# Kernel optimization log

Measured on AMD Instinct MI355X. Metric: run time of the kernel, lower is better.

## Reference

```python
import jax, jax.numpy as jnp
import numpy as np

B, T, J = 8, 1024, 25
D_MODEL, D_STATE, D_CONV, EXPAND = 256, 16, 4, 2
D_INNER = EXPAND * D_MODEL            # 512
DT_RANK = (D_MODEL + 15) // 16        # 16
N_CLASSES = 60


def layernorm(x, g, b, eps=1e-5):
    mu = x.mean(-1, keepdims=True)
    var = ((x - mu) ** 2).mean(-1, keepdims=True)
    return (x - mu) * jax.lax.rsqrt(var + eps) * g + b


def selective_scan(u, delta, A, Bm, Cm, D):
    # u, delta: [b,l,d]; A: [d,n]; Bm, Cm: [b,l,n]; D: [d]
    dA = jnp.exp(delta[..., None] * A)                              # [b,l,d,n]
    dBu = delta[..., None] * Bm[:, :, None, :] * u[..., None]        # [b,l,d,n]

    def step(h, inp):
        dA_t, dBu_t, C_t = inp
        h = dA_t * h + dBu_t                                         # [b,d,n]
        y = jnp.einsum('bdn,bn->bd', h, C_t)
        return h, y

    h0 = jnp.zeros((u.shape[0], u.shape[2], A.shape[1]), u.dtype)
    _, ys = jax.lax.scan(step, h0, (jnp.moveaxis(dA, 1, 0),
                                    jnp.moveaxis(dBu, 1, 0),
                                    jnp.moveaxis(Cm, 1, 0)))
    return jnp.moveaxis(ys, 0, 1) + u * D                            # [b,l,d]


def setup_inputs() -> dict:
    key = jax.random.key(0)
    ks = jax.random.split(key, 12)
    rn = lambda k, s, sc=0.02: jax.random.normal(k, s, jnp.float32) * sc
    A_log = jnp.log(jnp.tile(jnp.arange(1, D_STATE + 1, dtype=jnp.float32), (D_INNER, 1)))
    return {
        'x': jax.random.normal(ks[0], (B, T, J, 3), jnp.float32),
        'embed_w': rn(ks[1], (D_MODEL, J * 9)), 'embed_b': jnp.zeros((D_MODEL,), jnp.float32),
        'pre_g': jnp.ones((D_MODEL,), jnp.float32), 'pre_b': jnp.zeros((D_MODEL,), jnp.float32),
        'in_proj_w': rn(ks[2], (2 * D_INNER, D_MODEL)),
        'conv_w': rn(ks[3], (D_INNER, 1, D_CONV)), 'conv_b': jnp.zeros((D_INNER,), jnp.float32),
        'x_proj_w': rn(ks[4], (DT_RANK + 2 * D_STATE, D_INNER)),
        'dt_proj_w': rn(ks[5], (D_INNER, DT_RANK)), 'dt_proj_b': rn(ks[6], (D_INNER,), 0.1),
        'A_log': A_log, 'D': jnp.ones((D_INNER,), jnp.float32),
        'out_proj_w': rn(ks[7], (D_MODEL, D_INNER)),
        'post_g': jnp.ones((D_MODEL,), jnp.float32), 'post_b': jnp.zeros((D_MODEL,), jnp.float32),
        'fine_w': rn(ks[8], (N_CLASSES, D_MODEL)), 'fine_b': jnp.zeros((N_CLASSES,), jnp.float32),
    }


def reference(x, embed_w, embed_b, pre_g, pre_b, in_proj_w, conv_w, conv_b,
              x_proj_w, dt_proj_w, dt_proj_b, A_log, D, out_proj_w,
              post_g, post_b, fine_w, fine_b):
    b, t = x.shape[0], x.shape[1]
    # --- SkeletonNormalizer: root-center (scale_joints=None) ---
    pos = x[..., :3] - x[:, :, 0:1, :3]                              # [B,T,J,3]
    # --- MotionFeatureBuilder: pos / vel / acc ---
    vel = jnp.concatenate([jnp.zeros_like(pos[:, :1]), pos[:, 1:] - pos[:, :-1]], axis=1)
    acc = jnp.concatenate([jnp.zeros_like(vel[:, :1]), vel[:, 1:] - vel[:, :-1]], axis=1)
    feat = jnp.concatenate([pos, vel, acc], axis=-1).reshape(b, t, -1)  # [B,T,J*9]
    # --- embed ---
    feat = feat @ embed_w.T + embed_b                                # [B,T,D_MODEL]
    # --- Mamba block on pre-norm, residual add ---
    hn = layernorm(feat, pre_g, pre_b)
    xz = hn @ in_proj_w.T                                            # [B,T,2*D_INNER]
    xm, res = jnp.split(xz, 2, axis=-1)
    # depthwise causal conv1d over time
    xm = jax.lax.conv_general_dilated(
        jnp.swapaxes(xm, 1, 2), conv_w, (1,), [(D_CONV - 1, 0)],
        dimension_numbers=('NCH', 'OIH', 'NCH'), feature_group_count=D_INNER)
    xm = jnp.swapaxes(xm + conv_b[None, :, None], 1, 2)              # [B,T,D_INNER]
    xm = jax.nn.silu(xm)
    dbl = xm @ x_proj_w.T                                            # [B,T,DT_RANK+2*D_STATE]
    dt = dbl[..., :DT_RANK]
    Bm = dbl[..., DT_RANK:DT_RANK + D_STATE]
    Cm = dbl[..., DT_RANK + D_STATE:]
    delta = jax.nn.softplus(dt @ dt_proj_w.T + dt_proj_b)            # [B,T,D_INNER]
    A = -jnp.exp(A_log)                                              # [D_INNER,D_STATE]
    y = selective_scan(xm, delta, A, Bm, Cm, D)
    y = y * jax.nn.silu(res)
    y = y @ out_proj_w.T                                             # [B,T,D_MODEL]
    feat = feat + y
    # --- post norm, mean pool, classify ---
    feat = layernorm(feat, post_g, post_b)
    pooled = feat.mean(axis=1)                                       # [B,D_MODEL]
    return pooled @ fine_w.T + fine_b                                # [B,N_CLASSES]
```

## Files before the change

kernel.cpp:

```cpp
#include <hip/hip_runtime.h>
#include <hip/hip_bf16.h>
#include <math.h>

#define Bb 8
#define Tt 1024
#define Jj 25
#define D_MODEL 256
#define D_STATE 16
#define D_CONV 4
#define D_INNER 512
#define DT_RANK 16
#define N_CLASSES 60
#define Mrows (Bb*Tt)
#define NC 64
#define CL 16

typedef unsigned short u16;
using bf16x8 = __attribute__((ext_vector_type(8))) __bf16;
using f32x4  = __attribute__((ext_vector_type(4))) float;

__device__ inline u16 f2bf(float x) {
    unsigned u = __float_as_uint(x);
    unsigned r = (u + 0x7fffu + ((u >> 16) & 1u)) >> 16;
    return (u16)r;
// ... 111 lines not shown
#pragma unroll
            for (int in = 0; in < 2; in++)
                acc[im][in] = mfma3(aH[im], aL[im], bH[in], bL[in], acc[im][in]);
    }

    float bias_c[2], g_c[2], b_c[2];
#pragma unroll
    for (int in = 0; in < 2; in++) {
        int gn = nb + in * 16 + fr;
        bias_c[in] = bias[gn];
        g_c[in] = g[gn];
        b_c[in] = b[gn];
    }
#pragma unroll
    for (int im = 0; im < 2; im++)
#pragma unroll
        for (int in = 0; in < 2; in++)
#pragma unroll
            for (int reg = 0; reg < 4; reg++) {
                float v = acc[im][in][reg] + bias_c[in];
                acc[im][in][reg] = v;
                int gm = m0 + im * 16 + quad * 4 + reg;
                int gn = nb + in * 16 + fr;
                feat[(long)gm * 256 + gn] = v;
            }
#pragma unroll
    for (int im = 0; im < 2; im++)
#pragma unroll
        for (int reg = 0; reg < 4; reg++) {
            float p = acc[im][0][reg] + acc[im][1][reg];
            p += __shfl_xor(p, 1);
            p += __shfl_xor(p, 2);
            p += __shfl_xor(p, 4);
            p += __shfl_xor(p, 8);
            if (fr == 0) red[(im * 16 + quad * 4 + reg) * 8 + wave] = p;
        }
    __syncthreads();
    if (tid < BM) {
        float s = 0.f;
#pragma unroll
        for (int i = 0; i < 8; i++) s += red[tid * 8 + i];
        mu_s[tid] = s * (1.f / 256.f);
    }
    __syncthreads();
#pragma unroll
    for (int im = 0; im < 2; im++)
#pragma unroll
        for (int reg = 0; reg < 4; reg++) {
            int rl = im * 16 + quad * 4 + reg;
            float m = mu_s[rl];
            float d0 = acc[im][0][reg] - m, d1 = acc[im][1][reg] - m;
            float p = d0 * d0 + d1 * d1;
            p += __shfl_xor(p, 1);
            p += __shfl_xor(p, 2);
            p += __shfl_xor(p, 4);
            p += __shfl_xor(p, 8);
            if (fr == 0) red[rl * 8 + wave] = p;
        }
    __syncthreads();
    if (tid < BM) {
        float s = 0.f;
#pragma unroll
        for (int i = 0; i < 8; i++) s += red[tid * 8 + i];
        rs_s[tid] = rsqrtf(s * (1.f / 256.f) + 1e-5f);
    }
    __syncthreads();
#pragma unroll
    for (int im = 0; im < 2; im++)
#pragma unroll
        for (int in = 0; in < 2; in++)
#pragma unroll
            for (int reg = 0; reg < 4; reg++) {
                int rl = im * 16 + quad * 4 + reg;
                int gm = m0 + rl;
                int gn = nb + in * 16 + fr;
                float o = (acc[im][in][reg] - mu_s[rl]) * rs_s[rl] * g_c[in] + b_c[in];
                u16 hh, ll;
                split2(o, hh, ll);
                hnh[(long)gm * 256 + gn] = hh;
                hnl[(long)gm * 256 + gn] = ll;
            }
}

__global__ __launch_bounds__(512) void outproj_ln_pool_kernel(
    const u16* __restrict__ Ahi, const u16* __restrict__ Alo,
    const u16* __restrict__ Whi, const u16* __restrict__ Wlo,
    const float* __restrict__ resid,
    const float* __restrict__ g, const float* __restrict__ b,
    float* __restrict__ bp)
{
    constexpr int BM = 32, SW = 520;
    __shared__ u16 AsH[BM * SW], AsL[BM * SW];
    __shared__ float red[BM * 8];
    __shared__ float mu_s[BM], rs_s[BM];
    int tid = threadIdx.x;
    int m0 = blockIdx.x * BM;
    int lane = tid & 63, wave = tid >> 6;
    int fr = lane & 15, quad = lane >> 4;

    for (int s = tid; s < BM * 64; s += 512) {
        int row = s >> 6, seg = s & 63;
        long off = (long)(m0 + row) * 512 + seg * 8;
        *(uint4*)&AsH[row * SW + seg * 8] = *(const uint4*)(Ahi + off);
        *(uint4*)&AsL[row * SW + seg * 8] = *(const uint4*)(Alo + off);
    }
    __syncthreads();

    f32x4 acc[2][2] = {};
    int nb = wave * 32;
#pragma unroll 4
    for (int k0 = 0; k0 < 512; k0 += 32) {
        bf16x8 aH[2], aL[2], bH[2], bL[2];
#pragma unroll
        for (int im = 0; im < 2; im++) {
            int r = im * 16 + fr;
            aH[im] = *(const bf16x8*)&AsH[r * SW + k0 + quad * 8];
            aL[im] = *(const bf16x8*)&AsL[r * SW + k0 + quad * 8];
        }
#pragma unroll
        for (int in = 0; in < 2; in++) {
            long off = (long)(nb + in * 16 + fr) * 512 + k0 + quad * 8;
            bH[in] = *(const bf16x8*)(Whi + off);
            bL[in] = *(const bf16x8*)(Wlo + off);
        }
#pragma unroll
        for (int im = 0; im < 2; im++)
#pragma unroll
            for (int in = 0; in < 2; in++)
                acc[im][in] = mfma3(aH[im], aL[im], bH[in], bL[in], acc[im][in]);
    }

    float g_c[2], b_c[2];
#pragma unroll
    for (int in = 0; in < 2; in++) {
        int gn = nb + in * 16 + fr;
        g_c[in] = g[gn];
        b_c[in] = b[gn];
    }
#pragma unroll
    for (int im = 0; im < 2; im++)
#pragma unroll
        for (int in = 0; in < 2; in++)
#pragma unroll
            for (int reg = 0; reg < 4; reg++) {
                int gm = m0 + im * 16 + quad * 4 + reg;
                int gn = nb + in * 16 + fr;
                acc[im][in][reg] += resid[(long)gm * 256 + gn];
            }
#pragma unroll
    for (int im = 0; im < 2; im++)
#pragma unroll
        for (int reg = 0; reg < 4; reg++) {
            float p = acc[im][0][reg] + acc[im][1][reg];
            p += __shfl_xor(p, 1);
            p += __shfl_xor(p, 2);
            p += __shfl_xor(p, 4);
            p += __shfl_xor(p, 8);
            if (fr == 0) red[(im * 16 + quad * 4 + reg) * 8 + wave] = p;
        }
    __syncthreads();
    if (tid < BM) {
        float s = 0.f;
#pragma unroll
        for (int i = 0; i < 8; i++) s += red[tid * 8 + i];
        mu_s[tid] = s * (1.f / 256.f);
    }
    __syncthreads();
#pragma unroll
    for (int im = 0; im < 2; im++)
#pragma unroll
        for (int reg = 0; reg < 4; reg++) {
            int rl = im * 16 + quad * 4 + reg;
            float m = mu_s[rl];
            float d0 = acc[im][0][reg] - m, d1 = acc[im][1][reg] - m;
            float p = d0 * d0 + d1 * d1;
            p += __shfl_xor(p, 1);
            p += __shfl_xor(p, 2);
            p += __shfl_xor(p, 4);
            p += __shfl_xor(p, 8);
            if (fr == 0) red[rl * 8 + wave] = p;
        }
    __syncthreads();
    if (tid < BM) {
        float s = 0.f;
#pragma unroll
        for (int i = 0; i < 8; i++) s += red[tid * 8 + i];
        rs_s[tid] = rsqrtf(s * (1.f / 256.f) + 1e-5f);
    }
    __syncthreads();
#pragma unroll
    for (int in = 0; in < 2; in++) {
        float cs = 0.f;
#pragma unroll
        for (int im = 0; im < 2; im++)
#pragma unroll
            for (int reg = 0; reg < 4; reg++) {
                int rl = im * 16 + quad * 4 + reg;
                cs += (acc[im][in][reg] - mu_s[rl]) * rs_s[rl] * g_c[in] + b_c[in];
            }
        cs += __shfl_xor(cs, 16);
        cs += __shfl_xor(cs, 32);
        if (quad == 0) {
            int gn = nb + in * 16 + fr;
            atomicAdd(&bp[(long)(m0 >> 6) * 256 + gn], cs);
        }
    }
}

template<int BM, int BN, int EPI>
__global__ __launch_bounds__(256) void gemm_mfma(
    const u16* __restrict__ Ahi, const u16* __restrict__ Alo, int lda,
    const u16* __restrict__ Whi, const u16* __restrict__ Wlo, int ldw,
    const float* __restrict__ bias, const float* __restrict__ resid, int ldr,
    float* __restrict__ C, int ldc, int M, int N, int K)
{
    constexpr int TM = BM / 32;
    constexpr int TN = BN / 32;
    constexpr int SA = 40;
    __shared__ u16 AsH[BM * SA], AsL[BM * SA];
    __shared__ u16 WsH[BN * SA], WsL[BN * SA];
    int tid = threadIdx.x;
    int m0 = blockIdx.y * BM;
    int n0 = blockIdx.x * BN;
    int lane = tid & 63;
    int wave = tid >> 6;
    int wm = wave >> 1, wn = wave & 1;
    int fr = lane & 15, quad = lane >> 4;
    f32x4 acc[TM][TN] = {};

    for (int k0 = 0; k0 < K; k0 += 32) {
        for (int s = tid; s < BM * 4; s += 256) {
            int row = s >> 2, seg = s & 3;
            long off = (long)(m0 + row) * lda + k0 + seg * 8;
            *(uint4*)&AsH[row * SA + seg * 8] = *(const uint4*)(Ahi + off);
            *(uint4*)&AsL[row * SA + seg * 8] = *(const uint4*)(Alo + off);
        }
        for (int s = tid; s < BN * 4; s += 256) {
            int row = s >> 2, seg = s & 3;
            long off = (long)(n0 + row) * ldw + k0 + seg * 8;
            *(uint4*)&WsH[row * SA + seg * 8] = *(const uint4*)(Whi + off);
            *(uint4*)&WsL[row * SA + seg * 8] = *(const uint4*)(Wlo + off);
        }
        __syncthreads();
        bf16x8 aH[TM], aL[TM], bH[TN], bL[TN];
#pragma unroll
        for (int im = 0; im < TM; im++) {
            int r = wm * (BM / 2) + im * 16 + fr;
            aH[im] = *(const bf16x8*)&AsH[r * SA + quad * 8];
            aL[im] = *(const bf16x8*)&AsL[r * SA + quad * 8];
        }
#pragma unroll
        for (int in = 0; in < TN; in++) {
            int r = wn * (BN / 2) + in * 16 + fr;
            bH[in] = *(const bf16x8*)&WsH[r * SA + quad * 8];
            bL[in] = *(const bf16x8*)&WsL[r * SA + quad * 8];
        }
#pragma unroll
        for (int im = 0; im < TM; im++)
#pragma unroll
            for (int in = 0; in < TN; in++)
                acc[im][in] = mfma3(aH[im], aL[im], bH[in], bL[in], acc[im][in]);
        __syncthreads();
    }
#pragma unroll
    for (int im = 0; im < TM; im++) {
#pragma unroll
        for (int in = 0; in < TN; in++) {
#pragma unroll
            for (int reg = 0; reg < 4; reg++) {
                int gm = m0 + wm * (BM / 2) + im * 16 + quad * 4 + reg;
                int gn = n0 + wn * (BN / 2) + in * 16 + fr;
                float v = acc[im][in][reg];
                if (EPI == 1) v += bias[gn];
                if (EPI == 3) v += resid[(long)gm * ldr + gn];
                C[(long)gm * ldc + gn] = v;
            }
        }
    }
}

__global__ __launch_bounds__(512) void scan_p1f(
    const float* __restrict__ xz,
    const float* __restrict__ cw, const float* __restrict__ cb,
    const u16* __restrict__ Whi, const u16* __restrict__ Wlo,
    const float* __restrict__ dtw, const float* __restrict__ dtb,
    const float* __restrict__ A_log,
    float* __restrict__ chunkS, float* __restrict__ sumdelta)
{
    constexpr int SW = 520;
    __shared__ u16 AsH[CL * SW], AsL[CL * SW];
    __shared__ float ds[CL * 48];
    int b = blockIdx.x, c = blockIdx.y, d = threadIdx.x;
    int lane = d & 63, wave = d >> 6;
    int fr = lane & 15, quad = lane >> 4;
    long r0 = (long)b * Tt + (long)c * CL;
    int t0 = c * CL;

    float4 w4 = *(const float4*)(cw + d * 4);
    float cbd = cb[d];
    const float* xc = xz + r0 * 1024 + d;
    float h1 = (t0 >= 1) ? xc[-1024] : 0.f;
    float h2 = (t0 >= 2) ? xc[-2048] : 0.f;
    float h3 = (t0 >= 3) ? xc[-3072] : 0.f;
#pragma unroll
    for (int t = 0; t < CL; t++) {
        float cur = xc[t * 1024];
        float a = cbd + w4.w * cur + w4.z * h1 + w4.y * h2 + w4.x * h3;
        float s = a / (1.f + __expf(-a));
        u16 hh, ll;
        split2(s, hh, ll);
        AsH[t * SW + d] = hh;
        AsL[t * SW + d] = ll;
        h3 = h2; h2 = h1; h1 = cur;
    }
    float Arow[16];
#pragma unroll
    for (int n = 0; n < 16; n++) Arow[n] = -expf(A_log[d * 16 + n]);
    float4 wd[4];
#pragma unroll
    for (int q = 0; q < 4; q++) wd[q] = *(const float4*)(dtw + d * 16 + q * 4);
    float bdt = dtb[d];
    __syncthreads();

    if (wave < 3) {
        f32x4 acc = {};
#pragma unroll
        for (int k0 = 0; k0 < 512; k0 += 32) {
            bf16x8 aH = *(const bf16x8*)&AsH[fr * SW + k0 + quad * 8];
            bf16x8 aL = *(const bf16x8*)&AsL[fr * SW + k0 + quad * 8];
            long off = (long)(wave * 16 + fr) * 512 + k0 + quad * 8;
            bf16x8 bH = *(const bf16x8*)(Whi + off);
            bf16x8 bL = *(const bf16x8*)(Wlo + off);
            acc = mfma3(aH, aL, bH, bL, acc);
        }
#pragma unroll
        for (int reg = 0; reg < 4; reg++)
            ds[(quad * 4 + reg) * 48 + wave * 16 + fr] = acc[reg];
    }
    __syncthreads();

    float S[16];
#pragma unroll
    for (int n = 0; n < 16; n++) S[n] = 0.f;
    float sd = 0.f;
    for (int t = 0; t < CL; t++) {
        const float* row = ds + t * 48;
        float4 t1 = *(const float4*)(row + 0);
        float4 t2 = *(const float4*)(row + 4);
        float4 t3 = *(const float4*)(row + 8);
        float4 t4 = *(const float4*)(row + 12);
        float s = bdt;
        s += t1.x * wd[0].x + t1.y * wd[0].y + t1.z * wd[0].z + t1.w * wd[0].w;
        s += t2.x * wd[1].x + t2.y * wd[1].y + t2.z * wd[1].z + t2.w * wd[1].w;
        s += t3.x * wd[2].x + t3.y * wd[2].y + t3.z * wd[2].z + t3.w * wd[2].w;
        s += t4.x * wd[3].x + t4.y * wd[3].y + t4.z * wd[3].z + t4.w * wd[3].w;
        float dl = softplus_fast(s);
        float u = bf2f(AsH[t * SW + d]) + bf2f(AsL[t * SW + d]);
        float du = dl * u;
        sd += dl;
        float Bn[16];
#pragma unroll
        for (int q = 0; q < 4; q++) {
            float4 bv = *(const float4*)(row + 16 + q * 4);
            Bn[q*4+0] = bv.x; Bn[q*4+1] = bv.y; Bn[q*4+2] = bv.z; Bn[q*4+3] = bv.w;
        }
#pragma unroll
        for (int n = 0; n < 16; n++) {
            float a = __expf(dl * Arow[n]);
            S[n] = a * S[n] + du * Bn[n];
        }
    }
    long base = ((long)(b * NC + c) * 16) * 512 + d;
#pragma unroll
    for (int n = 0; n < 16; n++) chunkS[base + (long)n * 512] = S[n];
    sumdelta[(long)(b * NC + c) * 512 + d] = sd;
}

__global__ __launch_bounds__(256) void scan_combine(float* chunkS,
                                                    const float* __restrict__ sumdelta,
                                                    const float* __restrict__ A_log) {
    int idx = blockIdx.x * 256 + threadIdx.x;
    int d = idx & 511;
    int n = (idx >> 9) & 15;
    int b = idx >> 13;
    float Aval = -expf(A_log[d * 16 + n]);
    float h = 0.f;
    for (int c = 0; c < NC; c++) {
        long si = ((long)(b * NC + c) * 16 + n) * 512 + d;
        float s = chunkS[si];
        float a = __expf(Aval * sumdelta[(long)(b * NC + c) * 512 + d]);
        chunkS[si] = h;
        h = a * h + s;
    }
}

__global__ __launch_bounds__(512) void scan_p2f(
    const float* __restrict__ xz,
    const float* __restrict__ cw, const float* __restrict__ cb,
    const u16* __restrict__ Whi, const u16* __restrict__ Wlo,
    const float* __restrict__ dtw, const float* __restrict__ dtb,
    const float* __restrict__ A_log, const float* __restrict__ Dv,
    const float* __restrict__ chunkH,
    u16* __restrict__ yh, u16* __restrict__ yl)
{
    constexpr int SW = 520;
    __shared__ u16 AsH[CL * SW], AsL[CL * SW];
    __shared__ float ds[CL * 48];
    int b = blockIdx.x, c = blockIdx.y, d = threadIdx.x;
    int lane = d & 63, wave = d >> 6;
    int fr = lane & 15, quad = lane >> 4;
    long r0 = (long)b * Tt + (long)c * CL;
    int t0 = c * CL;

    float4 w4 = *(const float4*)(cw + d * 4);
    float cbd = cb[d];
    const float* xc = xz + r0 * 1024 + d;
    float h1 = (t0 >= 1) ? xc[-1024] : 0.f;
    float h2 = (t0 >= 2) ? xc[-2048] : 0.f;
    float h3 = (t0 >= 3) ? xc[-3072] : 0.f;
#pragma unroll
    for (int t = 0; t < CL; t++) {
        float cur = xc[t * 1024];
        float a = cbd + w4.w * cur + w4.z * h1 + w4.y * h2 + w4.x * h3;
        float s = a / (1.f + __expf(-a));
        u16 hh, ll;
        split2(s, hh, ll);
        AsH[t * SW + d] = hh;
        AsL[t * SW + d] = ll;
        h3 = h2; h2 = h1; h1 = cur;
    }
    float Arow[16];
#pragma unroll
    for (int n = 0; n < 16; n++) Arow[n] = -expf(A_log[d * 16 + n]);
    float4 wd[4];
#pragma unroll
    for (int q = 0; q < 4; q++) wd[q] = *(const float4*)(dtw + d * 16 + q * 4);
    float bdt = dtb[d];
    float Dd = Dv[d];
    float h[16];
    long base = ((long)(b * NC + c) * 16) * 512 + d;
#pragma unroll
    for (int n = 0; n < 16; n++) h[n] = chunkH[base + (long)n * 512];
    __syncthreads();

    if (wave < 3) {
        f32x4 acc = {};
#pragma unroll
        for (int k0 = 0; k0 < 512; k0 += 32) {
            bf16x8 aH = *(const bf16x8*)&AsH[fr * SW + k0 + quad * 8];
            bf16x8 aL = *(const bf16x8*)&AsL[fr * SW + k0 + quad * 8];
            long off = (long)(wave * 16 + fr) * 512 + k0 + quad * 8;
            bf16x8 bH = *(const bf16x8*)(Whi + off);
            bf16x8 bL = *(const bf16x8*)(Wlo + off);
            acc = mfma3(aH, aL, bH, bL, acc);
        }
#pragma unroll
        for (int reg = 0; reg < 4; reg++)
            ds[(quad * 4 + reg) * 48 + wave * 16 + fr] = acc[reg];
    }
    __syncthreads();

    const float* xres = xz + r0 * 1024 + 512 + d;
    for (int t = 0; t < CL; t++) {
        const float* row = ds + t * 48;
        float4 t1 = *(const float4*)(row + 0);
        float4 t2 = *(const float4*)(row + 4);
        float4 t3 = *(const float4*)(row + 8);
        float4 t4 = *(const float4*)(row + 12);
        float s = bdt;
        s += t1.x * wd[0].x + t1.y * wd[0].y + t1.z * wd[0].z + t1.w * wd[0].w;
        s += t2.x * wd[1].x + t2.y * wd[1].y + t2.z * wd[1].z + t2.w * wd[1].w;
        s += t3.x * wd[2].x + t3.y * wd[2].y + t3.z * wd[2].z + t3.w * wd[2].w;
        s += t4.x * wd[3].x + t4.y * wd[3].y + t4.z * wd[3].z + t4.w * wd[3].w;
        float dl = softplus_fast(s);
        float u = bf2f(AsH[t * SW + d]) + bf2f(AsL[t * SW + d]);
        float res = xres[t * 1024];
        float du = dl * u;
        float Bn[16], Cn[16];
#pragma unroll
        for (int q = 0; q < 4; q++) {
            float4 bv = *(const float4*)(row + 16 + q * 4);
            float4 cv = *(const float4*)(row + 32 + q * 4);
            Bn[q*4+0] = bv.x; Bn[q*4+1] = bv.y; Bn[q*4+2] = bv.z; Bn[q*4+3] = bv.w;
            Cn[q*4+0] = cv.x; Cn[q*4+1] = cv.y; Cn[q*4+2] = cv.z; Cn[q*4+3] = cv.w;
        }
        float ysum = 0.f;
#pragma unroll
        for (int n = 0; n < 16; n++) {
            float a = __expf(dl * Arow[n]);
            h[n] = a * h[n] + du * Bn[n];
            ysum += h[n] * Cn[n];
        }
        float yy = ysum + u * Dd;
        float sres = res / (1.f + __expf(-res));
        float outv = yy * sres;
        u16 hh, ll;
        split2(outv, hh, ll);
        long r = r0 + t;
        yh[r * 512 + d] = hh;
        yl[r * 512 + d] = ll;
    }
}

__global__ __launch_bounds__(256) void head_kernel(const float* __restrict__ bp,
                                                   const float* __restrict__ fw,
                                                   const float* __restrict__ fb,
                                                   float* __restrict__ out) {
    __shared__ float pld[256];
    int b = blockIdx.x;
    int d = threadIdx.x;
    float s = 0.f;
#pragma unroll
    for (int i = 0; i < 16; i++)
        s += bp[(long)(b * 16 + i) * 256 + d];
    pld[d] = s;
    __syncthreads();
    if (d < N_CLASSES) {
        float acc = 0.f;
        for (int k = 0; k < 256; k++) acc += pld[k] * fw[d * 256 + k];
        out[b * N_CLASSES + d] = acc * (1.f / (float)Tt) + fb[d];
    }
}

extern "C" void kernel_launch(void* const* d_in, const int* in_sizes, int n_in,
                              void* d_out, int out_size, void* d_ws, size_t ws_size,
                              hipStream_t stream) {
    const float* x         = (const float*)d_in[0];
    const float* embed_w   = (const float*)d_in[1];
    const float* embed_b   = (const float*)d_in[2];
    const float* pre_g     = (const float*)d_in[3];
    const float* pre_b     = (const float*)d_in[4];
    const float* in_proj_w = (const float*)d_in[5];
    const float* conv_w    = (const float*)d_in[6];
    const float* conv_b    = (const float*)d_in[7];
    const float* x_proj_w  = (const float*)d_in[8];
    const float* dt_proj_w = (const float*)d_in[9];
    const float* dt_proj_b = (const float*)d_in[10];
    const float* A_log     = (const float*)d_in[11];
    const float* Dv        = (const float*)d_in[12];
    const float* out_proj_w= (const float*)d_in[13];
    const float* post_g    = (const float*)d_in[14];
    const float* post_b    = (const float*)d_in[15];
    const float* fine_w    = (const float*)d_in[16];
    const float* fine_b    = (const float*)d_in[17];
    float* out = (float*)d_out;
    char* base = (char*)d_ws;

    float* feat     = (float*)(base + 0);
    float* xz       = (float*)(base + 8388608);
    float* chunkS   = (float*)(base + 41943040);
    u16*   xmh      = (u16*)  (base + 58720256);
    u16*   xml      = (u16*)  (base + 67108864);
    u16*   fbh      = (u16*)  (base + 75497472);
    u16*   fbl      = (u16*)  (base + 79691776);
    float* sumdelta = (float*)(base + 85458944);
    float* blockpart= (float*)(base + 86507520);
    u16*   ebh      = (u16*)  (base + 86638592);
    u16*   ebl      = ebh + 65536;
    u16*   iph      = ebl + 65536;
    u16*   ipl      = iph + 262144;
    u16*   xph      = ipl + 262144;
    u16*   xpl      = xph + 24576;
    u16*   oph      = xpl + 24576;
    u16*   opl      = oph + 131072;

    prep_kernel<<<dim3(1888 + 128), dim3(256), 0, stream>>>(
        embed_w, in_proj_w, x_proj_w, out_proj_w,
        ebh, ebl, iph, ipl, xph, xpl, oph, opl, blockpart);

    embed_ln_kernel<<<dim3(Mrows / 32), dim3(512), 0, stream>>>(
        x, ebh, ebl, embed_b, pre_g, pre_b, feat, fbh, fbl);

    gemm_mfma<128,64,0><<<dim3(16, 64), dim3(256), 0, stream>>>(
        fbh, fbl, 256, iph, ipl, 256, nullptr, nullptr, 0, xz, 1024, Mrows, 1024, 256);

    scan_p1f<<<dim3(Bb, NC), dim3(512), 0, stream>>>(
        xz, conv_w, conv_b, xph, xpl, dt_proj_w, dt_proj_b, A_log,
        chunkS, sumdelta);
    scan_combine<<<dim3(256), dim3(256), 0, stream>>>(chunkS, sumdelta, A_log);
    scan_p2f<<<dim3(Bb, NC), dim3(512), 0, stream>>>(
        xz, conv_w, conv_b, xph, xpl, dt_proj_w, dt_proj_b, A_log, Dv,
        chunkS, xmh, xml);

    outproj_ln_pool_kernel<<<dim3(Mrows / 32), dim3(512), 0, stream>>>(
        xmh, xml, oph, opl, feat, post_g, post_b, blockpart);

    head_kernel<<<dim3(Bb), dim3(256), 0, stream>>>(blockpart, fine_w, fine_b, out);
}
```

Before: 236.0 us.

## Replace generic in_proj GEMM with full-K A-tile kernel streaming weights from global

Swaps the templated tiled GEMM for in_proj for a dedicated kernel. Each block loads a 64x256 activation tile (hi and lo bf16 halves) into LDS once, with a single barrier. Waves then read weight fragments straight from global memory, which removes the per-K-step LDS staging and the syncs between steps. The weights are small and likely cache-resident. The risk is that the global weight loads sit on the MFMA critical path without prefetching, and the larger LDS footprint limits occupancy.

```diff
diff --git a/kernel.cpp b/kernel.cpp
--- a/kernel.cpp
+++ b/kernel.cpp
@@ -217,6 +217,63 @@
             }
 }
 
+__global__ __launch_bounds__(512, 2) void inproj_kernel(
+    const u16* __restrict__ Ahi, const u16* __restrict__ Alo,
+    const u16* __restrict__ Whi, const u16* __restrict__ Wlo,
+    float* __restrict__ xz)
+{
+    constexpr int BM = 64, SW = 264;
+    __shared__ u16 AsH[BM * SW], AsL[BM * SW];
+    int tid = threadIdx.x;
+    int n0 = blockIdx.x * 256;
+    int m0 = blockIdx.y * BM;
+    int lane = tid & 63, wave = tid >> 6;
+    int fr = lane & 15, quad = lane >> 4;
+
+    for (int s = tid; s < BM * 32; s += 512) {
+        int row = s >> 5, seg = s & 31;
+        long off = (long)(m0 + row) * 256 + seg * 8;
+        *(uint4*)&AsH[row * SW + seg * 8] = *(const uint4*)(Ahi + off);
+        *(uint4*)&AsL[row * SW + seg * 8] = *(const uint4*)(Alo + off);
+    }
+    __syncthreads();
+
+    f32x4 acc[4][2] = {};
+    int nb = n0 + wave * 32;
+#pragma unroll
+    for (int k0 = 0; k0 < 256; k0 += 32) {
+        bf16x8 aH[4], aL[4], bH[2], bL[2];
+#pragma unroll
+        for (int im = 0; im < 4; im++) {
+            int r = im * 16 + fr;
+            aH[im] = *(const bf16x8*)&AsH[r * SW + k0 + quad * 8];
+            aL[im] = *(const bf16x8*)&AsL[r * SW + k0 + quad * 8];
+        }
+#pragma unroll
+        for (int in = 0; in < 2; in++) {
+            long off = (long)(nb + in * 16 + fr) * 256 + k0 + quad * 8;
+            bH[in] = *(const bf16x8*)(Whi + off);
+            bL[in] = *(const bf16x8*)(Wlo + off);
+        }
+#pragma unroll
+        for (int im = 0; im < 4; im++)
+#pragma unroll
+            for (int in = 0; in < 2; in++)
+                acc[im][in] = mfma3(aH[im], aL[im], bH[in], bL[in], acc[im][in]);
+    }
+
+#pragma unroll
+    for (int im = 0; im < 4; im++)
+#pragma unroll
+        for (int in = 0; in < 2; in++)
+#pragma unroll
+            for (int reg = 0; reg < 4; reg++) {
+                int gm = m0 + im * 16 + quad * 4 + reg;
+                int gn = nb + in * 16 + fr;
+                xz[(long)gm * 1024 + gn] = acc[im][in][reg];
+            }
+}
+
 __global__ __launch_bounds__(512) void outproj_ln_pool_kernel(
     const u16* __restrict__ Ahi, const u16* __restrict__ Alo,
     const u16* __restrict__ Whi, const u16* __restrict__ Wlo,
@@ -338,78 +395,6 @@
         if (quad == 0) {
             int gn = nb + in * 16 + fr;
             atomicAdd(&bp[(long)(m0 >> 6) * 256 + gn], cs);
-        }
-    }
-}
-
-template<int BM, int BN, int EPI>
-__global__ __launch_bounds__(256) void gemm_mfma(
-    const u16* __restrict__ Ahi, const u16* __restrict__ Alo, int lda,
-    const u16* __restrict__ Whi, const u16* __restrict__ Wlo, int ldw,
-    const float* __restrict__ bias, const float* __restrict__ resid, int ldr,
-    float* __restrict__ C, int ldc, int M, int N, int K)
-{
-    constexpr int TM = BM / 32;
-    constexpr int TN = BN / 32;
-    constexpr int SA = 40;
-    __shared__ u16 AsH[BM * SA], AsL[BM * SA];
-    __shared__ u16 WsH[BN * SA], WsL[BN * SA];
-    int tid = threadIdx.x;
-    int m0 = blockIdx.y * BM;
-    int n0 = blockIdx.x * BN;
-    int lane = tid & 63;
-    int wave = tid >> 6;
-    int wm = wave >> 1, wn = wave & 1;
-    int fr = lane & 15, quad = lane >> 4;
-    f32x4 acc[TM][TN] = {};
-
-    for (int k0 = 0; k0 < K; k0 += 32) {
-        for (int s = tid; s < BM * 4; s += 256) {
-            int row = s >> 2, seg = s & 3;
-            long off = (long)(m0 + row) * lda + k0 + seg * 8;
-            *(uint4*)&AsH[row * SA + seg * 8] = *(const uint4*)(Ahi + off);
-            *(uint4*)&AsL[row * SA + seg * 8] = *(const uint4*)(Alo + off);
-        }
-        for (int s = tid; s < BN * 4; s += 256) {
-            int row = s >> 2, seg = s & 3;
-            long off = (long)(n0 + row) * ldw + k0 + seg * 8;
-            *(uint4*)&WsH[row * SA + seg * 8] = *(const uint4*)(Whi + off);
-            *(uint4*)&WsL[row * SA + seg * 8] = *(const uint4*)(Wlo + off);
-        }
-        __syncthreads();
-        bf16x8 aH[TM], aL[TM], bH[TN], bL[TN];
-#pragma unroll
-        for (int im = 0; im < TM; im++) {
-            int r = wm * (BM / 2) + im * 16 + fr;
-            aH[im] = *(const bf16x8*)&AsH[r * SA + quad * 8];
-            aL[im] = *(const bf16x8*)&AsL[r * SA + quad * 8];
-        }
-#pragma unroll
-        for (int in = 0; in < TN; in++) {
-            int r = wn * (BN / 2) + in * 16 + fr;
-            bH[in] = *(const bf16x8*)&WsH[r * SA + quad * 8];
-            bL[in] = *(const bf16x8*)&WsL[r * SA + quad * 8];
-        }
-#pragma unroll
-        for (int im = 0; im < TM; im++)
-#pragma unroll
-            for (int in = 0; in < TN; in++)
-                acc[im][in] = mfma3(aH[im], aL[im], bH[in], bL[in], acc[im][in]);
-        __syncthreads();
-    }
-#pragma unroll
-    for (int im = 0; im < TM; im++) {
-#pragma unroll
-        for (int in = 0; in < TN; in++) {
-#pragma unroll
-            for (int reg = 0; reg < 4; reg++) {
-                int gm = m0 + wm * (BM / 2) + im * 16 + quad * 4 + reg;
-                int gn = n0 + wn * (BN / 2) + in * 16 + fr;
-                float v = acc[im][in][reg];
-                if (EPI == 1) v += bias[gn];
-                if (EPI == 3) v += resid[(long)gm * ldr + gn];
-                C[(long)gm * ldc + gn] = v;
-            }
         }
     }
 }
@@ -706,8 +691,8 @@
     embed_ln_kernel<<<dim3(Mrows / 32), dim3(512), 0, stream>>>(
         x, ebh, ebl, embed_b, pre_g, pre_b, feat, fbh, fbl);
 
-    gemm_mfma<128,64,0><<<dim3(16, 64), dim3(256), 0, stream>>>(
-        fbh, fbl, 256, iph, ipl, 256, nullptr, nullptr, 0, xz, 1024, Mrows, 1024, 256);
+    inproj_kernel<<<dim3(4, 128), dim3(512), 0, stream>>>(
+        fbh, fbl, iph, ipl, xz);
 
     scan_p1f<<<dim3(Bb, NC), dim3(512), 0, stream>>>(
         xz, conv_w, conv_b, xph, xpl, dt_proj_w, dt_proj_b, A_log,
```

New measurement: 242.5 us. 2.8% more time.

## Fuse out-projection, post layernorm and pooling into scan phase-2 kernel

Applied to the files above, without the earlier changes.

The scan second-phase kernel now writes its gated output (split into hi/lo bf16) into shared memory instead of global buffers. It then runs the out_proj MFMA GEMM, residual add, post layernorm and mean-pool atomics directly on its 16-row chunk. This removes a separate kernel launch and the global write and reread of the 8M-element split y tensor. The tradeoff is that each block has only 16 rows, so out_proj weights are reloaded from global by 512 blocks with less reuse per load. The GEMM also runs serialized after the scan inside each block.

```diff
diff --git a/kernel.cpp b/kernel.cpp
--- a/kernel.cpp
+++ b/kernel.cpp
@@ -217,131 +217,6 @@
             }
 }
 
-__global__ __launch_bounds__(512) void outproj_ln_pool_kernel(
-    const u16* __restrict__ Ahi, const u16* __restrict__ Alo,
-    const u16* __restrict__ Whi, const u16* __restrict__ Wlo,
-    const float* __restrict__ resid,
-    const float* __restrict__ g, const float* __restrict__ b,
-    float* __restrict__ bp)
-{
-    constexpr int BM = 32, SW = 520;
-    __shared__ u16 AsH[BM * SW], AsL[BM * SW];
-    __shared__ float red[BM * 8];
-    __shared__ float mu_s[BM], rs_s[BM];
-    int tid = threadIdx.x;
-    int m0 = blockIdx.x * BM;
-    int lane = tid & 63, wave = tid >> 6;
-    int fr = lane & 15, quad = lane >> 4;
-
-    for (int s = tid; s < BM * 64; s += 512) {
-        int row = s >> 6, seg = s & 63;
-        long off = (long)(m0 + row) * 512 + seg * 8;
-        *(uint4*)&AsH[row * SW + seg * 8] = *(const uint4*)(Ahi + off);
-        *(uint4*)&AsL[row * SW + seg * 8] = *(const uint4*)(Alo + off);
-    }
-    __syncthreads();
-
-    f32x4 acc[2][2] = {};
-    int nb = wave * 32;
-#pragma unroll 4
-    for (int k0 = 0; k0 < 512; k0 += 32) {
-        bf16x8 aH[2], aL[2], bH[2], bL[2];
-#pragma unroll
-        for (int im = 0; im < 2; im++) {
-            int r = im * 16 + fr;
-            aH[im] = *(const bf16x8*)&AsH[r * SW + k0 + quad * 8];
-            aL[im] = *(const bf16x8*)&AsL[r * SW + k0 + quad * 8];
-        }
-#pragma unroll
-        for (int in = 0; in < 2; in++) {
-            long off = (long)(nb + in * 16 + fr) * 512 + k0 + quad * 8;
-            bH[in] = *(const bf16x8*)(Whi + off);
-            bL[in] = *(const bf16x8*)(Wlo + off);
-        }
-#pragma unroll
-        for (int im = 0; im < 2; im++)
-#pragma unroll
-            for (int in = 0; in < 2; in++)
-                acc[im][in] = mfma3(aH[im], aL[im], bH[in], bL[in], acc[im][in]);
-    }
-
-    float g_c[2], b_c[2];
-#pragma unroll
-    for (int in = 0; in < 2; in++) {
-        int gn = nb + in * 16 + fr;
-        g_c[in] = g[gn];
-        b_c[in] = b[gn];
-    }
-#pragma unroll
-    for (int im = 0; im < 2; im++)
-#pragma unroll
-        for (int in = 0; in < 2; in++)
-#pragma unroll
-            for (int reg = 0; reg < 4; reg++) {
-                int gm = m0 + im * 16 + quad * 4 + reg;
-                int gn = nb + in * 16 + fr;
-                acc[im][in][reg] += resid[(long)gm * 256 + gn];
-            }
-#pragma unroll
-    for (int im = 0; im < 2; im++)
-#pragma unroll
-        for (int reg = 0; reg < 4; reg++) {
-            float p = acc[im][0][reg] + acc[im][1][reg];
-            p += __shfl_xor(p, 1);
-            p += __shfl_xor(p, 2);
-            p += __shfl_xor(p, 4);
-            p += __shfl_xor(p, 8);
-            if (fr == 0) red[(im * 16 + quad * 4 + reg) * 8 + wave] = p;
-        }
-    __syncthreads();
-    if (tid < BM) {
-        float s = 0.f;
-#pragma unroll
-        for (int i = 0; i < 8; i++) s += red[tid * 8 + i];
-        mu_s[tid] = s * (1.f / 256.f);
-    }
-    __syncthreads();
-#pragma unroll
-    for (int im = 0; im < 2; im++)
-#pragma unroll
-        for (int reg = 0; reg < 4; reg++) {
-            int rl = im * 16 + quad * 4 + reg;
-            float m = mu_s[rl];
-            float d0 = acc[im][0][reg] - m, d1 = acc[im][1][reg] - m;
-            float p = d0 * d0 + d1 * d1;
-            p += __shfl_xor(p, 1);
-            p += __shfl_xor(p, 2);
-            p += __shfl_xor(p, 4);
-            p += __shfl_xor(p, 8);
-            if (fr == 0) red[rl * 8 + wave] = p;
-        }
-    __syncthreads();
-    if (tid < BM) {
-        float s = 0.f;
-#pragma unroll
-        for (int i = 0; i < 8; i++) s += red[tid * 8 + i];
-        rs_s[tid] = rsqrtf(s * (1.f / 256.f) + 1e-5f);
-    }
-    __syncthreads();
-#pragma unroll
-    for (int in = 0; in < 2; in++) {
-        float cs = 0.f;
-#pragma unroll
-        for (int im = 0; im < 2; im++)
-#pragma unroll
-            for (int reg = 0; reg < 4; reg++) {
-                int rl = im * 16 + quad * 4 + reg;
-                cs += (acc[im][in][reg] - mu_s[rl]) * rs_s[rl] * g_c[in] + b_c[in];
-            }
-        cs += __shfl_xor(cs, 16);
-        cs += __shfl_xor(cs, 32);
-        if (quad == 0) {
-            int gn = nb + in * 16 + fr;
-            atomicAdd(&bp[(long)(m0 >> 6) * 256 + gn], cs);
-        }
-    }
-}
-
 template<int BM, int BN, int EPI>
 __global__ __launch_bounds__(256) void gemm_mfma(
     const u16* __restrict__ Ahi, const u16* __restrict__ Alo, int lda,
@@ -529,18 +404,23 @@
     }
 }
 
-__global__ __launch_bounds__(512) void scan_p2f(
+__global__ __launch_bounds__(512) void scan_p2_fused(
     const float* __restrict__ xz,
     const float* __restrict__ cw, const float* __restrict__ cb,
     const u16* __restrict__ Whi, const u16* __restrict__ Wlo,
     const float* __restrict__ dtw, const float* __restrict__ dtb,
     const float* __restrict__ A_log, const float* __restrict__ Dv,
     const float* __restrict__ chunkH,
-    u16* __restrict__ yh, u16* __restrict__ yl)
+    const u16* __restrict__ Ohi, const u16* __restrict__ Olo,
+    const float* __restrict__ resid,
+    const float* __restrict__ g, const float* __restrict__ b_,
+    float* __restrict__ bp)
 {
     constexpr int SW = 520;
     __shared__ u16 AsH[CL * SW], AsL[CL * SW];
     __shared__ float ds[CL * 48];
+    __shared__ float red[CL * 8];
+    __shared__ float mu_s[CL], rs_s[CL];
     int b = blockIdx.x, c = blockIdx.y, d = threadIdx.x;
     int lane = d & 63, wave = d >> 6;
     int fr = lane & 15, quad = lane >> 4;
@@ -573,9 +453,9 @@
     float bdt = dtb[d];
     float Dd = Dv[d];
     float h[16];
-    long base = ((long)(b * NC + c) * 16) * 512 + d;
-#pragma unroll
-    for (int n = 0; n < 16; n++) h[n] = chunkH[base + (long)n * 512];
+    long hbase = ((long)(b * NC + c) * 16) * 512 + d;
+#pragma unroll
+    for (int n = 0; n < 16; n++) h[n] = chunkH[hbase + (long)n * 512];
     __syncthreads();
 
     if (wave < 3) {
@@ -631,9 +511,92 @@
         float outv = yy * sres;
         u16 hh, ll;
         split2(outv, hh, ll);
-        long r = r0 + t;
-        yh[r * 512 + d] = hh;
-        yl[r * 512 + d] = ll;
+        AsH[t * SW + d] = hh;
+        AsL[t * SW + d] = ll;
+    }
+    __syncthreads();
+
+    f32x4 acc[2] = {};
+    int nb = wave * 32;
+#pragma unroll 4
+    for (int k0 = 0; k0 < 512; k0 += 32) {
+        bf16x8 aH = *(const bf16x8*)&AsH[fr * SW + k0 + quad * 8];
+        bf16x8 aL = *(const bf16x8*)&AsL[fr * SW + k0 + quad * 8];
+#pragma unroll
+        for (int in = 0; in < 2; in++) {
+            long off = (long)(nb + in * 16 + fr) * 512 + k0 + quad * 8;
+            bf16x8 bH = *(const bf16x8*)(Ohi + off);
+            bf16x8 bL = *(const bf16x8*)(Olo + off);
+            acc[in] = mfma3(aH, aL, bH, bL, acc[in]);
+        }
+    }
+
+    float g_c[2], b_c[2];
+#pragma unroll
+    for (int in = 0; in < 2; in++) {
+        int gn = nb + in * 16 + fr;
+        g_c[in] = g[gn];
+        b_c[in] = b_[gn];
+    }
+#pragma unroll
+    for (int in = 0; in < 2; in++)
+#pragma unroll
+        for (int reg = 0; reg < 4; reg++) {
+            long gm = r0 + quad * 4 + reg;
+            int gn = nb + in * 16 + fr;
+            acc[in][reg] += resid[gm * 256 + gn];
+        }
+#pragma unroll
+    for (int reg = 0; reg < 4; reg++) {
+        float p = acc[0][reg] + acc[1][reg];
+        p += __shfl_xor(p, 1);
+        p += __shfl_xor(p, 2);
+        p += __shfl_xor(p, 4);
+        p += __shfl_xor(p, 8);
+        if (fr == 0) red[(quad * 4 + reg) * 8 + wave] = p;
+    }
+    __syncthreads();
+    if (d < CL) {
+        float s = 0.f;
+#pragma unroll
+        for (int i = 0; i < 8; i++) s += red[d * 8 + i];
+        mu_s[d] = s * (1.f / 256.f);
+    }
+    __syncthreads();
+#pragma unroll
+    for (int reg = 0; reg < 4; reg++) {
+        int rl = quad * 4 + reg;
+        float m = mu_s[rl];
+        float d0 = acc[0][reg] - m, d1 = acc[1][reg] - m;
+        float p = d0 * d0 + d1 * d1;
+        p += __shfl_xor(p, 1);
+        p += __shfl_xor(p, 2);
+        p += __shfl_xor(p, 4);
+        p += __shfl_xor(p, 8);
+        if (fr == 0) red[rl * 8 + wave] = p;
+    }
+    __syncthreads();
+    if (d < CL) {
+        float s = 0.f;
+#pragma unroll
+        for (int i = 0; i < 8; i++) s += red[d * 8 + i];
+        rs_s[d] = rsqrtf(s * (1.f / 256.f) + 1e-5f);
+    }
+    __syncthreads();
+#pragma unroll
+    for (int in = 0; in < 2; in++) {
+        float cs = 0.f;
+#pragma unroll
+        for (int reg = 0; reg < 4; reg++) {
+            int rl = quad * 4 + reg;
+            cs += (acc[in][reg] - mu_s[rl]) * rs_s[rl] * g_c[in] + b_c[in];
+        }
+        cs += __shfl_xor(cs, 16);
+        cs += __shfl_xor(cs, 32);
+        if (quad == 0) {
+            int gn = nb + in * 16 + fr;
+            atomicAdd(&bp[(long)(r0 >> 6) * 256 + gn], cs);
+        }
     }
 }
 
@@ -684,8 +647,6 @@
     float* feat     = (float*)(base + 0);
     float* xz       = (float*)(base + 8388608);
     float* chunkS   = (float*)(base + 41943040);
-    u16*   xmh      = (u16*)  (base + 58720256);
-    u16*   xml      = (u16*)  (base + 67108864);
     u16*   fbh      = (u16*)  (base + 75497472);
     u16*   fbl      = (u16*)  (base + 79691776);
     float* sumdelta = (float*)(base + 85458944);
@@ -713,12 +674,10 @@
         xz, conv_w, conv_b, xph, xpl, dt_proj_w, dt_proj_b, A_log,
         chunkS, sumdelta);
     scan_combine<<<dim3(256), dim3(256), 0, stream>>>(chunkS, sumdelta, A_log);
-    scan_p2f<<<dim3(Bb, NC), dim3(512), 0, stream>>>(
+
+    scan_p2_fused<<<dim3(Bb, NC), dim3(512), 0, stream>>>(
         xz, conv_w, conv_b, xph, xpl, dt_proj_w, dt_proj_b, A_log, Dv,
-        chunkS, xmh, xml);
-
-    outproj_ln_pool_kernel<<<dim3(Mrows / 32), dim3(512), 0, stream>>>(
-        xmh, xml, oph, opl, feat, post_g, post_b, blockpart);
+        chunkS, oph, opl, feat, post_g, post_b, blockpart);
 
     head_kernel<<<dim3(Bb), dim3(256), 0, stream>>>(blockpart, fine_w, fine_b, out);
 }
```

After: 241.6 us. +2.4%, slower.

## Store conv output, delta and B/C in scan pass 1 and reuse them in pass 2

Applied to the files above, without the earlier changes.

Scan pass 1 now writes the conv+silu output (hi/lo bf16), the softplus delta and the B/C projections to global memory. Pass 2 becomes a lighter kernel that reads these back instead of recomputing the conv, the x_proj MFMA and the dt projection. This trades repeated compute for extra global traffic: about 16 MB of delta and 16 MB of conv output are written and then read again. The conv output is staged in the xmh/xml buffers and overwritten in place by y. The outproj kernel is only moved within the file.

```diff
diff --git a/kernel.cpp b/kernel.cpp
--- a/kernel.cpp
+++ b/kernel.cpp
@@ -217,131 +217,6 @@
             }
 }
 
-__global__ __launch_bounds__(512) void outproj_ln_pool_kernel(
-    const u16* __restrict__ Ahi, const u16* __restrict__ Alo,
-    const u16* __restrict__ Whi, const u16* __restrict__ Wlo,
-    const float* __restrict__ resid,
-    const float* __restrict__ g, const float* __restrict__ b,
-    float* __restrict__ bp)
-{
-    constexpr int BM = 32, SW = 520;
-    __shared__ u16 AsH[BM * SW], AsL[BM * SW];
-    __shared__ float red[BM * 8];
-    __shared__ float mu_s[BM], rs_s[BM];
-    int tid = threadIdx.x;
-    int m0 = blockIdx.x * BM;
-    int lane = tid & 63, wave = tid >> 6;
-    int fr = lane & 15, quad = lane >> 4;
-
-    for (int s = tid; s < BM * 64; s += 512) {
-        int row = s >> 6, seg = s & 63;
-        long off = (long)(m0 + row) * 512 + seg * 8;
-        *(uint4*)&AsH[row * SW + seg * 8] = *(const uint4*)(Ahi + off);
-        *(uint4*)&AsL[row * SW + seg * 8] = *(const uint4*)(Alo + off);
-    }
-    __syncthreads();
-
-    f32x4 acc[2][2] = {};
-    int nb = wave * 32;
-#pragma unroll 4
-    for (int k0 = 0; k0 < 512; k0 += 32) {
-        bf16x8 aH[2], aL[2], bH[2], bL[2];
-#pragma unroll
-        for (int im = 0; im < 2; im++) {
-            int r = im * 16 + fr;
-            aH[im] = *(const bf16x8*)&AsH[r * SW + k0 + quad * 8];
-            aL[im] = *(const bf16x8*)&AsL[r * SW + k0 + quad * 8];
-        }
-#pragma unroll
-        for (int in = 0; in < 2; in++) {
-            long off = (long)(nb + in * 16 + fr) * 512 + k0 + quad * 8;
-            bH[in] = *(const bf16x8*)(Whi + off);
-            bL[in] = *(const bf16x8*)(Wlo + off);
-        }
-#pragma unroll
-        for (int im = 0; im < 2; im++)
-#pragma unroll
-            for (int in = 0; in < 2; in++)
-                acc[im][in] = mfma3(aH[im], aL[im], bH[in], bL[in], acc[im][in]);
-    }
-
-    float g_c[2], b_c[2];
-#pragma unroll
-    for (int in = 0; in < 2; in++) {
-        int gn = nb + in * 16 + fr;
-        g_c[in] = g[gn];
-        b_c[in] = b[gn];
-    }
-#pragma unroll
-    for (int im = 0; im < 2; im++)
-#pragma unroll
-        for (int in = 0; in < 2; in++)
-#pragma unroll
-            for (int reg = 0; reg < 4; reg++) {
-                int gm = m0 + im * 16 + quad * 4 + reg;
-                int gn = nb + in * 16 + fr;
-                acc[im][in][reg] += resid[(long)gm * 256 + gn];
-            }
-#pragma unroll
-    for (int im = 0; im < 2; im++)
-#pragma unroll
-        for (int reg = 0; reg < 4; reg++) {
-            float p = acc[im][0][reg] + acc[im][1][reg];
-            p += __shfl_xor(p, 1);
-            p += __shfl_xor(p, 2);
-            p += __shfl_xor(p, 4);
-            p += __shfl_xor(p, 8);
-            if (fr == 0) red[(im * 16 + quad * 4 + reg) * 8 + wave] = p;
-        }
-    __syncthreads();
-    if (tid < BM) {
-        float s = 0.f;
-#pragma unroll
-        for (int i = 0; i < 8; i++) s += red[tid * 8 + i];
-        mu_s[tid] = s * (1.f / 256.f);
-    }
-    __syncthreads();
-#pragma unroll
-    for (int im = 0; im < 2; im++)
-#pragma unroll
-        for (int reg = 0; reg < 4; reg++) {
-            int rl = im * 16 + quad * 4 + reg;
-            float m = mu_s[rl];
-            float d0 = acc[im][0][reg] - m, d1 = acc[im][1][reg] - m;
-            float p = d0 * d0 + d1 * d1;
-            p += __shfl_xor(p, 1);
-            p += __shfl_xor(p, 2);
-            p += __shfl_xor(p, 4);
-            p += __shfl_xor(p, 8);
-            if (fr == 0) red[rl * 8 + wave] = p;
-        }
-    __syncthreads();
-    if (tid < BM) {
-        float s = 0.f;
-#pragma unroll
-        for (int i = 0; i < 8; i++) s += red[tid * 8 + i];
-        rs_s[tid] = rsqrtf(s * (1.f / 256.f) + 1e-5f);
-    }
-    __syncthreads();
-#pragma unroll
-    for (int in = 0; in < 2; in++) {
-        float cs = 0.f;
-#pragma unroll
-        for (int im = 0; im < 2; im++)
-#pragma unroll
-            for (int reg = 0; reg < 4; reg++) {
-                int rl = im * 16 + quad * 4 + reg;
-                cs += (acc[im][in][reg] - mu_s[rl]) * rs_s[rl] * g_c[in] + b_c[in];
-            }
-        cs += __shfl_xor(cs, 16);
-        cs += __shfl_xor(cs, 32);
-        if (quad == 0) {
-            int gn = nb + in * 16 + fr;
-            atomicAdd(&bp[(long)(m0 >> 6) * 256 + gn], cs);
-        }
-    }
-}
-
 template<int BM, int BN, int EPI>
 __global__ __launch_bounds__(256) void gemm_mfma(
     const u16* __restrict__ Ahi, const u16* __restrict__ Alo, int lda,
@@ -420,7 +295,9 @@
     const u16* __restrict__ Whi, const u16* __restrict__ Wlo,
     const float* __restrict__ dtw, const float* __restrict__ dtb,
     const float* __restrict__ A_log,
-    float* __restrict__ chunkS, float* __restrict__ sumdelta)
+    float* __restrict__ chunkS, float* __restrict__ sumdelta,
+    u16* __restrict__ uh, u16* __restrict__ ul,
+    float* __restrict__ dls, float* __restrict__ bc)
 {
     constexpr int SW = 520;
     __shared__ u16 AsH[CL * SW], AsL[CL * SW];
@@ -446,6 +323,8 @@
         split2(s, hh, ll);
         AsH[t * SW + d] = hh;
         AsL[t * SW + d] = ll;
+        uh[(r0 + t) * 512 + d] = hh;
+        ul[(r0 + t) * 512 + d] = ll;
         h3 = h2; h2 = h1; h1 = cur;
     }
     float Arow[16];
@@ -473,6 +352,8 @@
             ds[(quad * 4 + reg) * 48 + wave * 16 + fr] = acc[reg];
     }
     __syncthreads();
+
+    bc[r0 * 32 + d] = ds[(d >> 5) * 48 + 16 + (d & 31)];
 
     float S[16];
 #pragma unroll
@@ -490,6 +371,7 @@
         s += t3.x * wd[2].x + t3.y * wd[2].y + t3.z * wd[2].z + t3.w * wd[2].w;
         s += t4.x * wd[3].x + t4.y * wd[3].y + t4.z * wd[3].z + t4.w * wd[3].w;
         float dl = softplus_fast(s);
+        dls[(r0 + t) * 512 + d] = dl;
         float u = bf2f(AsH[t * SW + d]) + bf2f(AsL[t * SW + d]);
         float du = dl * u;
         sd += dl;
@@ -529,93 +411,42 @@
     }
 }
 
-__global__ __launch_bounds__(512) void scan_p2f(
+__global__ __launch_bounds__(512) void scan_p2l(
+    const float* __restrict__ bc,
+    const float* __restrict__ dls,
     const float* __restrict__ xz,
-    const float* __restrict__ cw, const float* __restrict__ cb,
-    const u16* __restrict__ Whi, const u16* __restrict__ Wlo,
-    const float* __restrict__ dtw, const float* __restrict__ dtb,
     const float* __restrict__ A_log, const float* __restrict__ Dv,
     const float* __restrict__ chunkH,
     u16* __restrict__ yh, u16* __restrict__ yl)
 {
-    constexpr int SW = 520;
-    __shared__ u16 AsH[CL * SW], AsL[CL * SW];
-    __shared__ float ds[CL * 48];
+    __shared__ float bcs[CL * 32];
     int b = blockIdx.x, c = blockIdx.y, d = threadIdx.x;
-    int lane = d & 63, wave = d >> 6;
-    int fr = lane & 15, quad = lane >> 4;
     long r0 = (long)b * Tt + (long)c * CL;
-    int t0 = c * CL;
-
-    float4 w4 = *(const float4*)(cw + d * 4);
-    float cbd = cb[d];
-    const float* xc = xz + r0 * 1024 + d;
-    float h1 = (t0 >= 1) ? xc[-1024] : 0.f;
-    float h2 = (t0 >= 2) ? xc[-2048] : 0.f;
-    float h3 = (t0 >= 3) ? xc[-3072] : 0.f;
-#pragma unroll
-    for (int t = 0; t < CL; t++) {
-        float cur = xc[t * 1024];
-        float a = cbd + w4.w * cur + w4.z * h1 + w4.y * h2 + w4.x * h3;
-        float s = a / (1.f + __expf(-a));
-        u16 hh, ll;
-        split2(s, hh, ll);
-        AsH[t * SW + d] = hh;
-        AsL[t * SW + d] = ll;
-        h3 = h2; h2 = h1; h1 = cur;
-    }
+
+    bcs[d] = bc[r0 * 32 + d];
     float Arow[16];
 #pragma unroll
     for (int n = 0; n < 16; n++) Arow[n] = -expf(A_log[d * 16 + n]);
-    float4 wd[4];
-#pragma unroll
-    for (int q = 0; q < 4; q++) wd[q] = *(const float4*)(dtw + d * 16 + q * 4);
-    float bdt = dtb[d];
     float Dd = Dv[d];
     float h[16];
-    long base = ((long)(b * NC + c) * 16) * 512 + d;
-#pragma unroll
-    for (int n = 0; n < 16; n++) h[n] = chunkH[base + (long)n * 512];
-    __syncthreads();
-
-    if (wave < 3) {
-        f32x4 acc = {};
-#pragma unroll
-        for (int k0 = 0; k0 < 512; k0 += 32) {
-            bf16x8 aH = *(const bf16x8*)&AsH[fr * SW + k0 + quad * 8];
-            bf16x8 aL = *(const bf16x8*)&AsL[fr * SW + k0 + quad * 8];
-            long off = (long)(wave * 16 + fr) * 512 + k0 + quad * 8;
-            bf16x8 bH = *(const bf16x8*)(Whi + off);
-            bf16x8 bL = *(const bf16x8*)(Wlo + off);
-            acc = mfma3(aH, aL, bH, bL, acc);
-        }
-#pragma unroll
-        for (int reg = 0; reg < 4; reg++)
-            ds[(quad * 4 + reg) * 48 + wave * 16 + fr] = acc[reg];
-    }
+    long hbase = ((long)(b * NC + c) * 16) * 512 + d;
+#pragma unroll
+    for (int n = 0; n < 16; n++) h[n] = chunkH[hbase + (long)n * 512];
     __syncthreads();
 
     const float* xres = xz + r0 * 1024 + 512 + d;
     for (int t = 0; t < CL; t++) {
-        const float* row = ds + t * 48;
-        float4 t1 = *(const float4*)(row + 0);
-        float4 t2 = *(const float4*)(row + 4);
-        float4 t3 = *(const float4*)(row + 8);
-        float4 t4 = *(const float4*)(row + 12);
-        float s = bdt;
-        s += t1.x * wd[0].x + t1.y * wd[0].y + t1.z * wd[0].z + t1.w * wd[0].w;
-        s += t2.x * wd[1].x + t2.y * wd[1].y + t2.z * wd[1].z + t2.w * wd[1].w;
-        s += t3.x * wd[2].x + t3.y * wd[2].y + t3.z * wd[2].z + t3.w * wd[2].w;
-        s += t4.x * wd[3].x + t4.y * wd[3].y + t4.z * wd[3].z + t4.w * wd[3].w;
-        float dl = softplus_fast(s);
-        float u = bf2f(AsH[t * SW + d]) + bf2f(AsL[t * SW + d]);
+        long r = r0 + t;
+        float dl = dls[r * 512 + d];
+        float u = bf2f(yh[r * 512 + d]) + bf2f(yl[r * 512 + d]);
         float res = xres[t * 1024];
         float du = dl * u;
+        const float* row = bcs + t * 32;
         float Bn[16], Cn[16];
 #pragma unroll
         for (int q = 0; q < 4; q++) {
-            float4 bv = *(const float4*)(row + 16 + q * 4);
-            float4 cv = *(const float4*)(row + 32 + q * 4);
+            float4 bv = *(const float4*)(row + q * 4);
+            float4 cv = *(const float4*)(row + 16 + q * 4);
             Bn[q*4+0] = bv.x; Bn[q*4+1] = bv.y; Bn[q*4+2] = bv.z; Bn[q*4+3] = bv.w;
             Cn[q*4+0] = cv.x; Cn[q*4+1] = cv.y; Cn[q*4+2] = cv.z; Cn[q*4+3] = cv.w;
         }
@@ -631,9 +462,133 @@
         float outv = yy * sres;
         u16 hh, ll;
         split2(outv, hh, ll);
-        long r = r0 + t;
         yh[r * 512 + d] = hh;
         yl[r * 512 + d] = ll;
+    }
+}
+
+__global__ __launch_bounds__(512) void outproj_ln_pool_kernel(
+    const u16* __restrict__ Ahi, const u16* __restrict__ Alo,
+    const u16* __restrict__ Whi, const u16* __restrict__ Wlo,
+    const float* __restrict__ resid,
+    const float* __restrict__ g, const float* __restrict__ b,
+    float* __restrict__ bp)
+{
+    constexpr int BM = 32, SW = 520;
+    __shared__ u16 AsH[BM * SW], AsL[BM * SW];
+    __shared__ float red[BM * 8];
+    __shared__ float mu_s[BM], rs_s[BM];
+    int tid = threadIdx.x;
+    int m0 = blockIdx.x * BM;
+    int lane = tid & 63, wave = tid >> 6;
+    int fr = lane & 15, quad = lane >> 4;
+
+    for (int s = tid; s < BM * 64; s += 512) {
+        int row = s >> 6, seg = s & 63;
+        long off = (long)(m0 + row) * 512 + seg * 8;
+        *(uint4*)&AsH[row * SW + seg * 8] = *(const uint4*)(Ahi + off);
+        *(uint4*)&AsL[row * SW + seg * 8] = *(const uint4*)(Alo + off);
+    }
+    __syncthreads();
+
+    f32x4 acc[2][2] = {};
+    int nb = wave * 32;
+#pragma unroll 4
+    for (int k0 = 0; k0 < 512; k0 += 32) {
+        bf16x8 aH[2], aL[2], bH[2], bL[2];
+#pragma unroll
+        for (int im = 0; im < 2; im++) {
+            int r = im * 16 + fr;
+            aH[im] = *(const bf16x8*)&AsH[r * SW + k0 + quad * 8];
+            aL[im] = *(const bf16x8*)&AsL[r * SW + k0 + quad * 8];
+        }
+#pragma unroll
+        for (int in = 0; in < 2; in++) {
+            long off = (long)(nb + in * 16 + fr) * 512 + k0 + quad * 8;
+            bH[in] = *(const bf16x8*)(Whi + off);
+            bL[in] = *(const bf16x8*)(Wlo + off);
+        }
+#pragma unroll
+        for (int im = 0; im < 2; im++)
+#pragma unroll
+            for (int in = 0; in < 2; in++)
+                acc[im][in] = mfma3(aH[im], aL[im], bH[in], bL[in], acc[im][in]);
+    }
+
+    float g_c[2], b_c[2];
+#pragma unroll
+    for (int in = 0; in < 2; in++) {
+        int gn = nb + in * 16 + fr;
+        g_c[in] = g[gn];
+        b_c[in] = b[gn];
+    }
+#pragma unroll
+    for (int im = 0; im < 2; im++)
+#pragma unroll
+        for (int in = 0; in < 2; in++)
+#pragma unroll
+            for (int reg = 0; reg < 4; reg++) {
+                int gm = m0 + im * 16 + quad * 4 + reg;
+                int gn = nb + in * 16 + fr;
+                acc[im][in][reg] += resid[(long)gm * 256 + gn];
+            }
+#pragma unroll
+    for (int im = 0; im < 2; im++)
+#pragma unroll
+        for (int reg = 0; reg < 4; reg++) {
+            float p = acc[im][0][reg] + acc[im][1][reg];
+            p += __shfl_xor(p, 1);
+            p += __shfl_xor(p, 2);
+            p += __shfl_xor(p, 4);
+            p += __shfl_xor(p, 8);
+            if (fr == 0) red[(im * 16 + quad * 4 + reg) * 8 + wave] = p;
+        }
+    __syncthreads();
+    if (tid < BM) {
+        float s = 0.f;
+#pragma unroll
+        for (int i = 0; i < 8; i++) s += red[tid * 8 + i];
+        mu_s[tid] = s * (1.f / 256.f);
+    }
+    __syncthreads();
+#pragma unroll
+    for (int im = 0; im < 2; im++)
+#pragma unroll
+        for (int reg = 0; reg < 4; reg++) {
+            int rl = im * 16 + quad * 4 + reg;
+            float m = mu_s[rl];
+            float d0 = acc[im][0][reg] - m, d1 = acc[im][1][reg] - m;
+            float p = d0 * d0 + d1 * d1;
+            p += __shfl_xor(p, 1);
+            p += __shfl_xor(p, 2);
+            p += __shfl_xor(p, 4);
+            p += __shfl_xor(p, 8);
+            if (fr == 0) red[rl * 8 + wave] = p;
+        }
+    __syncthreads();
+    if (tid < BM) {
+        float s = 0.f;
+#pragma unroll
+        for (int i = 0; i < 8; i++) s += red[tid * 8 + i];
+        rs_s[tid] = rsqrtf(s * (1.f / 256.f) + 1e-5f);
+    }
+    __syncthreads();
+#pragma unroll
+    for (int in = 0; in < 2; in++) {
+        float cs = 0.f;
+#pragma unroll
+        for (int im = 0; im < 2; im++)
+#pragma unroll
+            for (int reg = 0; reg < 4; reg++) {
+                int rl = im * 16 + quad * 4 + reg;
+                cs += (acc[im][in][reg] - mu_s[rl]) * rs_s[rl] * g_c[in] + b_c[in];
+            }
+        cs += __shfl_xor(cs, 16);
+        cs += __shfl_xor(cs, 32);
+        if (quad == 0) {
+            int gn = nb + in * 16 + fr;
+            atomicAdd(&bp[(long)(m0 >> 6) * 256 + gn], cs);
+        }
     }
 }
 
@@ -688,6 +643,7 @@
     u16*   xml      = (u16*)  (base + 67108864);
     u16*   fbh      = (u16*)  (base + 75497472);
     u16*   fbl      = (u16*)  (base + 79691776);
+    float* bc       = (float*)(base + 83886080);
     float* sumdelta = (float*)(base + 85458944);
     float* blockpart= (float*)(base + 86507520);
     u16*   ebh      = (u16*)  (base + 86638592);
@@ -698,6 +654,7 @@
     u16*   xpl      = xph + 24576;
     u16*   oph      = xpl + 24576;
     u16*   opl      = oph + 131072;
+    float* dls      = (float*)(base + 100663296);
 
     prep_kernel<<<dim3(1888 + 128), dim3(256), 0, stream>>>(
         embed_w, in_proj_w, x_proj_w, out_proj_w,
@@ -711,11 +668,11 @@
 
     scan_p1f<<<dim3(Bb, NC), dim3(512), 0, stream>>>(
         xz, conv_w, conv_b, xph, xpl, dt_proj_w, dt_proj_b, A_log,
-        chunkS, sumdelta);
+        chunkS, sumdelta, xmh, xml, dls, bc);
     scan_combine<<<dim3(256), dim3(256), 0, stream>>>(chunkS, sumdelta, A_log);
-    scan_p2f<<<dim3(Bb, NC), dim3(512), 0, stream>>>(
-        xz, conv_w, conv_b, xph, xpl, dt_proj_w, dt_proj_b, A_log, Dv,
-        chunkS, xmh, xml);
+
+    scan_p2l<<<dim3(Bb, NC), dim3(512), 0, stream>>>(
+        bc, dls, xz, A_log, Dv, chunkS, xmh, xml);
 
     outproj_ln_pool_kernel<<<dim3(Mrows / 32), dim3(512), 0, stream>>>(
         xmh, xml, oph, opl, feat, post_g, post_b, blockpart);
```

Result: no change. 231.5 us (-1.9%).
